# Performance work log

Hardware: AMD Instinct MI355X
Metric: run time of the kernel (lower is better)

The kernel has to match this reference:

```python
import math
import jax, jax.numpy as jnp
import numpy as np

B, S, HID = 2, 2048, 2048
H, D = 32, 64  # num heads, head dim (H*D == HID)


def setup_inputs() -> dict:
    key = jax.random.key(0)
    ks = jax.random.split(key, 5)
    scale = 1.0 / math.sqrt(HID)
    return {
        "hidden_states": jax.random.normal(ks[0], (B, S, HID), dtype=jnp.float32),
        "attention_mask": jnp.zeros((B, S), dtype=jnp.float32),
        "wq": jax.random.normal(ks[1], (HID, HID), dtype=jnp.float32) * scale,
        "wk": jax.random.normal(ks[2], (HID, HID), dtype=jnp.float32) * scale,
        "wv": jax.random.normal(ks[3], (HID, HID), dtype=jnp.float32) * scale,
        "wo": jax.random.normal(ks[4], (HID, HID), dtype=jnp.float32) * scale,
    }


def reference(hidden_states, attention_mask, wq, wk, wv, wo):
    b, s, _ = hidden_states.shape
    # QKV projections (nn.Linear stores weight as [out, in]; y = x @ W^T)
    q = (hidden_states @ wq.T).reshape(b, s, H, D).transpose(0, 2, 1, 3)  # [B,H,S,D]
    k = (hidden_states @ wk.T).reshape(b, s, H, D).transpose(0, 2, 1, 3)
    v = (hidden_states @ wv.T).reshape(b, s, H, D).transpose(0, 2, 1, 3)
    # rotary_emb_ is None in the source module, so no RoPE is applied.
    scores = jnp.einsum("bhqd,bhkd->bhqk", q, k) / math.sqrt(D)  # [B,H,S,S]
    scores = scores + attention_mask.reshape(b, 1, 1, s)  # additive mask
    probs = jax.nn.softmax(scores, axis=-1)
    ctx = jnp.einsum("bhqk,bhkd->bhqd", probs, v)  # [B,H,S,D]
    ctx = ctx.transpose(0, 2, 1, 3).reshape(b, s, H * D)  # [B,S,HID]
    return ctx @ wo.T
```

## Files before the change

### kernel.cpp

```cpp
#include <hip/hip_runtime.h>

using bf16x8 = __attribute__((ext_vector_type(8))) __bf16;
using f32x4  = __attribute__((ext_vector_type(4))) float;
using u16x8  = __attribute__((ext_vector_type(8))) unsigned short;

__device__ __forceinline__ unsigned short f2bf(float x) {
  unsigned int u = __float_as_uint(x);
  u += 0x7fffu + ((u >> 16) & 1u);
  return (unsigned short)(u >> 16);
}

__device__ __forceinline__ void gload16(const unsigned short* g, unsigned short* l) {
  __builtin_amdgcn_global_load_lds(
      (__attribute__((address_space(1))) void*)const_cast<unsigned short*>(g),
      (__attribute__((address_space(3))) void*)l, 16, 0, 0);
}

__global__ __launch_bounds__(256) void cvt_kernel(const float* __restrict__ in,
                                                  unsigned short* __restrict__ out) {
  const int i = blockIdx.x * 256 + threadIdx.x;
  const float4 v = ((const float4*)in)[i];
  ushort4 o;
  o.x = f2bf(v.x); o.y = f2bf(v.y); o.z = f2bf(v.z); o.w = f2bf(v.w);
  ((ushort4*)out)[i] = o;
}

template<int MODE>
__global__ __launch_bounds__(256)
void gemm_nt(const unsigned short* __restrict__ A,
             const unsigned short* __restrict__ Bw,
             float* __restrict__ Cf,
             unsigned short* __restrict__ Cq,
             int M, int N, int K)
{
  __shared__ unsigned short As[128 * 32];
  __shared__ unsigned short Bs[128 * 32];
  const int tid  = threadIdx.x;
  const int lane = tid & 63;
  const int wid  = tid >> 6;
  const int wr = wid >> 1, wc = wid & 1;
  const int lrow = lane & 15, lhi = lane >> 4;
  const int bn = blockIdx.x * 128;
  const int bm = blockIdx.y * 128;

  f32x4 acc[4][4] = {};

  const int srow = tid >> 2;
  const int scol = (tid & 3) * 8;
  const unsigned short* Ag0 = A  + (size_t)(bm + srow) * K + scol;
  const unsigned short* Ag1 = Ag0 + (size_t)64 * K;
  const unsigned short* Bg0 = Bw + (size_t)(bn + srow) * K + scol;
  const unsigned short* Bg1 = Bg0 + (size_t)64 * K;
  unsigned short* Ad0 = As + tid * 8;
  unsigned short* Ad1 = As + (256 + tid) * 8;
  unsigned short* Bd0 = Bs + tid * 8;
  unsigned short* Bd1 = Bs + (256 + tid) * 8;

  for (int k0 = 0; k0 < K; k0 += 32) {
    gload16(Ag0 + k0, Ad0);
    gload16(Ag1 + k0, Ad1);
    gload16(Bg0 + k0, Bd0);
    gload16(Bg1 + k0, Bd1);
    __syncthreads();
    bf16x8 af[4], bfr[4];
#pragma unroll
    for (int m = 0; m < 4; ++m)
      af[m] = *(const bf16x8*)(As + (wr * 64 + m * 16 + lrow) * 32 + lhi * 8);
#pragma unroll
    for (int n = 0; n < 4; ++n)
      bfr[n] = *(const bf16x8*)(Bs + (wc * 64 + n * 16 + lrow) * 32 + lhi * 8);
#pragma unroll
    for (int m = 0; m < 4; ++m)
#pragma unroll
      for (int n = 0; n < 4; ++n)
        acc[m][n] = __builtin_amdgcn_mfma_f32_16x16x32_bf16(af[m], bfr[n], acc[m][n], 0, 0, 0);
    __syncthreads();
  }

#pragma unroll
  for (int m = 0; m < 4; ++m) {
    const int row0 = bm + wr * 64 + m * 16 + lhi * 4;
#pragma unroll
    for (int n = 0; n < 4; ++n) {
      const int col = bn + wc * 64 + n * 16 + lrow;
#pragma unroll
      for (int r = 0; r < 4; ++r) {
        const int row = row0 + r;
        const float v = acc[m][n][r];
        if (MODE == 0) {
          const int which = col >> 11;
          const int h = (col >> 6) & 31;
          const int d = col & 63;
          const int b = row >> 11;
          const int s = row & 2047;
          Cq[(((size_t)which * 64 + b * 32 + h) * 2048 + s) * 64 + d] = f2bf(v);
        } else {
          Cf[(size_t)row * N + col] = v;
        }
      }
    }
  }
}

__global__ __launch_bounds__(256)
void attn_kernel(const unsigned short* __restrict__ QKV,
                 const float* __restrict__ mask,
                 unsigned short* __restrict__ Ctx)
{
  constexpr int S = 2048, D = 64, BH = 64;
  __shared__ unsigned short Klds[64 * 64];
  __shared__ unsigned short VT[64 * 64];
  __shared__ unsigned short Plds[4][16 * 64];
  __shared__ float mlds[64];

  const int tid  = threadIdx.x;
  const int lane = tid & 63;
  const int wid  = tid >> 6;
  const int lrow = lane & 15;
  const int lhi  = lane >> 4;
  const int bh = blockIdx.y;
  const int b  = bh >> 5;
  const int h  = bh & 31;
  const int qbase = blockIdx.x * 64;

  const size_t qoff = (size_t)bh * S * D;
  const size_t koff = qoff + (size_t)BH * S * D;
  const size_t voff = koff + (size_t)BH * S * D;

  bf16x8 qa[2];
  {
    const unsigned short* Qp = QKV + qoff + (size_t)(qbase + wid * 16 + lrow) * D + lhi * 8;
    qa[0] = *(const bf16x8*)(Qp);
    qa[1] = *(const bf16x8*)(Qp + 32);
  }

  f32x4 oacc[4] = {};
  float mrow[4] = {-1e30f, -1e30f, -1e30f, -1e30f};
  float srow[4] = {0.f, 0.f, 0.f, 0.f};

  const int krow = tid >> 3;
  const int kcol = (((tid & 7) ^ (krow & 7)) << 3);
  unsigned short* Kd0 = Klds + tid * 8;
  unsigned short* Kd1 = Klds + (256 + tid) * 8;

  const int vrow  = tid >> 2;
  const int vcol0 = (tid & 3) * 16;

  const float k1 = 0.125f * 1.44269504f;

  for (int t = 0; t < S / 64; ++t) {
    const int kb = t * 64;
    gload16(QKV + koff + (size_t)(kb + krow) * D + kcol, Kd0);
    gload16(QKV + koff + (size_t)(kb + 32 + krow) * D + kcol, Kd1);
    {
      const unsigned short* Vp = QKV + voff + (size_t)(kb + vrow) * D + vcol0;
      u16x8 v0 = *(const u16x8*)(Vp);
      u16x8 v1 = *(const u16x8*)(Vp + 8);
#pragma unroll
      for (int j = 0; j < 8; ++j) {
        const int dc = vcol0 + j;
        VT[dc * 64 + (((vrow >> 3) ^ (dc & 7) ^ (dc >> 4)) << 3) + (vrow & 7)] = v0[j];
      }
#pragma unroll
      for (int j = 0; j < 8; ++j) {
        const int dc = vcol0 + 8 + j;
        VT[dc * 64 + (((vrow >> 3) ^ (dc & 7) ^ (dc >> 4)) << 3) + (vrow & 7)] = v1[j];
      }
    }
    if (tid < 64) mlds[tid] = mask[(size_t)b * S + kb + tid] * 1.44269504f;
    __syncthreads();

    f32x4 sacc[4] = {};
#pragma unroll
    for (int f = 0; f < 4; ++f) {
      const int krw = f * 16 + lrow;
      bf16x8 kf0 = *(const bf16x8*)(Klds + krw * 64 + ((lhi ^ (lrow & 7)) << 3));
      bf16x8 kf1 = *(const bf16x8*)(Klds + krw * 64 + (((lhi + 4) ^ (lrow & 7)) << 3));
      sacc[f] = __builtin_amdgcn_mfma_f32_16x16x32_bf16(qa[0], kf0, sacc[f], 0, 0, 0);
      sacc[f] = __builtin_amdgcn_mfma_f32_16x16x32_bf16(qa[1], kf1, sacc[f], 0, 0, 0);
    }

    float pm[4] = {-1e30f, -1e30f, -1e30f, -1e30f};
#pragma unroll
    for (int f = 0; f < 4; ++f) {
      const float mk = mlds[lrow + 16 * f];
#pragma unroll
      for (int r = 0; r < 4; ++r) {
        float v = sacc[f][r] * k1 + mk;
        sacc[f][r] = v;
        pm[r] = fmaxf(pm[r], v);
      }
    }
#pragma unroll
    for (int off = 1; off < 16; off <<= 1)
#pragma unroll
      for (int r = 0; r < 4; ++r)
        pm[r] = fmaxf(pm[r], __shfl_xor(pm[r], off, 64));
#pragma unroll
    for (int r = 0; r < 4; ++r) {
      const float mnew  = fmaxf(mrow[r], pm[r]);
      const float alpha = exp2f(mrow[r] - mnew);
      mrow[r] = mnew;
      srow[r] *= alpha;
#pragma unroll
      for (int f = 0; f < 4; ++f) oacc[f][r] *= alpha;
      float ps = 0.f;
#pragma unroll
      for (int f = 0; f < 4; ++f) {
        const float p = exp2f(sacc[f][r] - mnew);
        sacc[f][r] = p;
        ps += p;
      }
      srow[r] += ps;
    }

    unsigned short* Pw = &Plds[wid][0];
#pragma unroll
    for (int f = 0; f < 4; ++f) {
      const int key = lrow + 16 * f;
#pragma unroll
      for (int r = 0; r < 4; ++r) {
        const int rho = lhi * 4 + r;
        Pw[rho * 64 + ((((key >> 3) ^ (rho & 7))) << 3) + (key & 7)] = f2bf(sacc[f][r]);
      }
    }

#pragma unroll
    for (int ks = 0; ks < 2; ++ks) {
      bf16x8 pa = *(const bf16x8*)(Pw + lrow * 64 + (((lhi + 4 * ks) ^ (lrow & 7)) << 3));
#pragma unroll
      for (int f = 0; f < 4; ++f) {
        const int dc = lrow + 16 * f;
        bf16x8 vb = *(const bf16x8*)(VT + dc * 64 + (((lhi + 4 * ks) ^ (dc & 7) ^ (dc >> 4)) << 3));
        oacc[f] = __builtin_amdgcn_mfma_f32_16x16x32_bf16(pa, vb, oacc[f], 0, 0, 0);
      }
    }
    __syncthreads();
  }

#pragma unroll
  for (int off = 1; off < 16; off <<= 1)
#pragma unroll
    for (int r = 0; r < 4; ++r)
      srow[r] += __shfl_xor(srow[r], off, 64);

#pragma unroll
  for (int f = 0; f < 4; ++f) {
    const int d = lrow + 16 * f;
#pragma unroll
    for (int r = 0; r < 4; ++r) {
      const int q = qbase + wid * 16 + lhi * 4 + r;
      const float v = oacc[f][r] / srow[r];
      Ctx[((size_t)b * S + q) * 2048 + h * 64 + d] = f2bf(v);
    }
  }
}

extern "C" void kernel_launch(void* const* d_in, const int* in_sizes, int n_in,
                              void* d_out, int out_size, void* d_ws, size_t ws_size,
                              hipStream_t stream) {
  const float* X    = (const float*)d_in[0];
  const float* mask = (const float*)d_in[1];
  const float* wq   = (const float*)d_in[2];
  const float* wk   = (const float*)d_in[3];
  const float* wv   = (const float*)d_in[4];
  const float* wo   = (const float*)d_in[5];

  unsigned short* ws   = (unsigned short*)d_ws;
  unsigned short* Xb   = ws;
  unsigned short* Wcat = Xb + 8388608;
  unsigned short* Wob  = Wcat + 12582912;
  unsigned short* QKVb = Wob + 4194304;
  unsigned short* Ctxb = QKVb + 25165824;

  cvt_kernel<<<8192, 256, 0, stream>>>(X, Xb);
  cvt_kernel<<<4096, 256, 0, stream>>>(wq, Wcat);
  cvt_kernel<<<4096, 256, 0, stream>>>(wk, Wcat + 4194304);
  cvt_kernel<<<4096, 256, 0, stream>>>(wv, Wcat + 8388608);
  cvt_kernel<<<4096, 256, 0, stream>>>(wo, Wob);

  gemm_nt<0><<<dim3(48, 32), 256, 0, stream>>>(Xb, Wcat, nullptr, QKVb, 4096, 6144, 2048);

  attn_kernel<<<dim3(32, 64), 256, 0, stream>>>(QKVb, mask, Ctxb);

  gemm_nt<1><<<dim3(16, 32), 256, 0, stream>>>(Ctxb, Wob, (float*)d_out, nullptr, 4096, 2048, 2048);
}
```

Before: 555.6 us.

## Double-buffer K/V tiles, store V transposed from QKV GEMM, use transpose LDS reads

The QKV projection epilogue now writes V in a transposed [bh][d][s] layout, so the attention kernel can load V tiles with direct global-to-LDS async copies instead of a per-element scatter transpose. K and V tiles are double-buffered so the next tile's loads are issued before the current tile is computed, and the per-tile barrier before compute is gone. The mask is read straight from global into registers, and P is packed with v_cvt_pk_bf16_f32 and read back through ds_read_b64_tr_b16. This adds LDS use and inline assembly with manual waitcnt. The transposed V store in the GEMM epilogue is strided and may be slower to write.

Result: slower. 572.5 us (+3.0%).

```diff
diff --git a/kernel.cpp b/kernel.cpp
--- a/kernel.cpp
+++ b/kernel.cpp
@@ -2,7 +2,7 @@
 
 using bf16x8 = __attribute__((ext_vector_type(8))) __bf16;
 using f32x4  = __attribute__((ext_vector_type(4))) float;
-using u16x8  = __attribute__((ext_vector_type(8))) unsigned short;
+using uint2v = __attribute__((ext_vector_type(2))) unsigned int;
 
 __device__ __forceinline__ unsigned short f2bf(float x) {
   unsigned int u = __float_as_uint(x);
@@ -93,7 +93,11 @@
           const int d = col & 63;
           const int b = row >> 11;
           const int s = row & 2047;
-          Cq[(((size_t)which * 64 + b * 32 + h) * 2048 + s) * 64 + d] = f2bf(v);
+          if (which == 2) {
+            Cq[(size_t)16777216 + ((size_t)(b * 32 + h) * 64 + d) * 2048 + s] = f2bf(v);
+          } else {
+            Cq[(((size_t)which * 64 + b * 32 + h) * 2048 + s) * 64 + d] = f2bf(v);
+          }
         } else {
           Cf[(size_t)row * N + col] = v;
         }
@@ -108,10 +112,9 @@
                  unsigned short* __restrict__ Ctx)
 {
   constexpr int S = 2048, D = 64, BH = 64;
-  __shared__ unsigned short Klds[64 * 64];
-  __shared__ unsigned short VT[64 * 64];
-  __shared__ unsigned short Plds[4][16 * 64];
-  __shared__ float mlds[64];
+  __shared__ unsigned short Klds[2][64 * 64];
+  __shared__ unsigned short Vlds[2][64 * 64];
+  __shared__ unsigned short PT[4][64 * 16];
 
   const int tid  = threadIdx.x;
   const int lane = tid & 63;
@@ -127,70 +130,67 @@
   const size_t koff = qoff + (size_t)BH * S * D;
   const size_t voff = koff + (size_t)BH * S * D;
 
-  bf16x8 qa[2];
+  bf16x8 qa0, qa1;
   {
     const unsigned short* Qp = QKV + qoff + (size_t)(qbase + wid * 16 + lrow) * D + lhi * 8;
-    qa[0] = *(const bf16x8*)(Qp);
-    qa[1] = *(const bf16x8*)(Qp + 32);
+    qa0 = *(const bf16x8*)Qp;
+    qa1 = *(const bf16x8*)(Qp + 32);
   }
 
   f32x4 oacc[4] = {};
   float mrow[4] = {-1e30f, -1e30f, -1e30f, -1e30f};
   float srow[4] = {0.f, 0.f, 0.f, 0.f};
 
-  const int krow = tid >> 3;
-  const int kcol = (((tid & 7) ^ (krow & 7)) << 3);
-  unsigned short* Kd0 = Klds + tid * 8;
-  unsigned short* Kd1 = Klds + (256 + tid) * 8;
-
-  const int vrow  = tid >> 2;
-  const int vcol0 = (tid & 3) * 16;
+  const int strow  = tid >> 3;
+  const int sswz   = ((tid & 7) ^ (strow & 7)) << 3;
+  const unsigned short* Kg = QKV + koff + (size_t)strow * D + sswz;
+  const unsigned short* Vg = QKV + voff + (size_t)strow * S + sswz;
 
   const float k1 = 0.125f * 1.44269504f;
+  const unsigned ptbase =
+      (unsigned)(uintptr_t)&PT[wid][0] + (unsigned)(lane * 8 + (lane >> 4) * 128);
+
+  auto stage = [&](int t, int c) {
+    const int kb = t * 64;
+    gload16(Kg + (size_t)kb * D,          &Klds[c][0] + tid * 8);
+    gload16(Kg + (size_t)kb * D + 32 * D, &Klds[c][0] + 2048 + tid * 8);
+    gload16(Vg + kb,                      &Vlds[c][0] + tid * 8);
+    gload16(Vg + kb + 32 * S,             &Vlds[c][0] + 2048 + tid * 8);
+  };
+
+  stage(0, 0);
+  __syncthreads();
 
   for (int t = 0; t < S / 64; ++t) {
-    const int kb = t * 64;
-    gload16(QKV + koff + (size_t)(kb + krow) * D + kcol, Kd0);
-    gload16(QKV + koff + (size_t)(kb + 32 + krow) * D + kcol, Kd1);
-    {
-      const unsigned short* Vp = QKV + voff + (size_t)(kb + vrow) * D + vcol0;
-      u16x8 v0 = *(const u16x8*)(Vp);
-      u16x8 v1 = *(const u16x8*)(Vp + 8);
-#pragma unroll
-      for (int j = 0; j < 8; ++j) {
-        const int dc = vcol0 + j;
-        VT[dc * 64 + (((vrow >> 3) ^ (dc & 7) ^ (dc >> 4)) << 3) + (vrow & 7)] = v0[j];
-      }
-#pragma unroll
-      for (int j = 0; j < 8; ++j) {
-        const int dc = vcol0 + 8 + j;
-        VT[dc * 64 + (((vrow >> 3) ^ (dc & 7) ^ (dc >> 4)) << 3) + (vrow & 7)] = v1[j];
-      }
-    }
-    if (tid < 64) mlds[tid] = mask[(size_t)b * S + kb + tid] * 1.44269504f;
-    __syncthreads();
-
+    const int kb  = t * 64;
+    const int cur = t & 1;
+    if (t + 1 < S / 64) stage(t + 1, cur ^ 1);
+
+    float mkl[4];
+#pragma unroll
+    for (int f = 0; f < 4; ++f)
+      mkl[f] = mask[(size_t)b * S + kb + lrow + 16 * f] * 1.44269504f;
+
+    const unsigned short* Kc = &Klds[cur][0];
     f32x4 sacc[4] = {};
 #pragma unroll
     for (int f = 0; f < 4; ++f) {
       const int krw = f * 16 + lrow;
-      bf16x8 kf0 = *(const bf16x8*)(Klds + krw * 64 + ((lhi ^ (lrow & 7)) << 3));
-      bf16x8 kf1 = *(const bf16x8*)(Klds + krw * 64 + (((lhi + 4) ^ (lrow & 7)) << 3));
-      sacc[f] = __builtin_amdgcn_mfma_f32_16x16x32_bf16(qa[0], kf0, sacc[f], 0, 0, 0);
-      sacc[f] = __builtin_amdgcn_mfma_f32_16x16x32_bf16(qa[1], kf1, sacc[f], 0, 0, 0);
+      bf16x8 kf0 = *(const bf16x8*)(Kc + krw * 64 + ((lhi ^ (lrow & 7)) << 3));
+      bf16x8 kf1 = *(const bf16x8*)(Kc + krw * 64 + (((lhi + 4) ^ (lrow & 7)) << 3));
+      sacc[f] = __builtin_amdgcn_mfma_f32_16x16x32_bf16(qa0, kf0, sacc[f], 0, 0, 0);
+      sacc[f] = __builtin_amdgcn_mfma_f32_16x16x32_bf16(qa1, kf1, sacc[f], 0, 0, 0);
     }
 
     float pm[4] = {-1e30f, -1e30f, -1e30f, -1e30f};
 #pragma unroll
-    for (int f = 0; f < 4; ++f) {
-      const float mk = mlds[lrow + 16 * f];
+    for (int f = 0; f < 4; ++f)
 #pragma unroll
       for (int r = 0; r < 4; ++r) {
-        float v = sacc[f][r] * k1 + mk;
+        const float v = sacc[f][r] * k1 + mkl[f];
         sacc[f][r] = v;
         pm[r] = fmaxf(pm[r], v);
       }
-    }
 #pragma unroll
     for (int off = 1; off < 16; off <<= 1)
 #pragma unroll
@@ -214,26 +214,37 @@
       srow[r] += ps;
     }
 
-    unsigned short* Pw = &Plds[wid][0];
+    unsigned short* PTw = &PT[wid][0];
 #pragma unroll
     for (int f = 0; f < 4; ++f) {
-      const int key = lrow + 16 * f;
-#pragma unroll
-      for (int r = 0; r < 4; ++r) {
-        const int rho = lhi * 4 + r;
-        Pw[rho * 64 + ((((key >> 3) ^ (rho & 7))) << 3) + (key & 7)] = f2bf(sacc[f][r]);
-      }
-    }
-
+      unsigned w0, w1;
+      asm("v_cvt_pk_bf16_f32 %0, %1, %2" : "=v"(w0) : "v"(sacc[f][0]), "v"(sacc[f][1]));
+      asm("v_cvt_pk_bf16_f32 %0, %1, %2" : "=v"(w1) : "v"(sacc[f][2]), "v"(sacc[f][3]));
+      uint2v w; w.x = w0; w.y = w1;
+      *(uint2v*)(PTw + (lrow + 16 * f) * 16 + lhi * 4) = w;
+    }
+
+    const unsigned short* Vc = &Vlds[cur][0];
 #pragma unroll
     for (int ks = 0; ks < 2; ++ks) {
-      bf16x8 pa = *(const bf16x8*)(Pw + lrow * 64 + (((lhi + 4 * ks) ^ (lrow & 7)) << 3));
+      uint2v r0, r1;
+      const unsigned a0 = ptbase + (unsigned)(ks * 1024);
+      asm volatile("ds_read_b64_tr_b16 %0, %1"            : "=v"(r0) : "v"(a0) : "memory");
+      asm volatile("ds_read_b64_tr_b16 %0, %1 offset:128" : "=v"(r1) : "v"(a0) : "memory");
+      bf16x8 vb[4];
 #pragma unroll
       for (int f = 0; f < 4; ++f) {
         const int dc = lrow + 16 * f;
-        bf16x8 vb = *(const bf16x8*)(VT + dc * 64 + (((lhi + 4 * ks) ^ (dc & 7) ^ (dc >> 4)) << 3));
-        oacc[f] = __builtin_amdgcn_mfma_f32_16x16x32_bf16(pa, vb, oacc[f], 0, 0, 0);
-      }
+        vb[f] = *(const bf16x8*)(Vc + dc * 64 + (((ks * 4 + lhi) ^ (dc & 7)) << 3));
+      }
+      asm volatile("s_waitcnt lgkmcnt(0)" ::: "memory");
+      __builtin_amdgcn_sched_barrier(0);
+      union { struct { uint2v a, b; } u; bf16x8 v; } pu;
+      pu.u.a = r0; pu.u.b = r1;
+      const bf16x8 pa = pu.v;
+#pragma unroll
+      for (int f = 0; f < 4; ++f)
+        oacc[f] = __builtin_amdgcn_mfma_f32_16x16x32_bf16(pa, vb[f], oacc[f], 0, 0, 0);
     }
     __syncthreads();
   }
```
